# Optimization experiments

Hardware: AMD Instinct MI355X
Metric: run time of the kernel (lower is better)

The kernel has to match this reference:

```python
import jax, jax.numpy as jnp
import numpy as np

D_MODEL = 1024
NUM_HEADS = 8
D_K = D_MODEL // NUM_HEADS
NEG_INF = -1e9
EPS = 1e-6


def setup_inputs() -> dict:
    key = jax.random.key(0)
    ks = jax.random.split(key, 10)
    B, S = 4, 2048
    scale = 1.0 / np.sqrt(D_MODEL)
    return {
        "queries": jax.random.normal(ks[0], (B, S, D_MODEL), jnp.float32),
        "keys": jax.random.normal(ks[1], (B, S, D_MODEL), jnp.float32),
        "values": jax.random.normal(ks[2], (B, S, D_MODEL), jnp.float32),
        "Wq": jax.random.normal(ks[3], (D_MODEL, D_MODEL), jnp.float32) * scale,
        "bq": jnp.zeros((D_MODEL,), jnp.float32),
        "Wk": jax.random.normal(ks[4], (D_MODEL, D_MODEL), jnp.float32) * scale,
        "bk": jnp.zeros((D_MODEL,), jnp.float32),
        "Wv": jax.random.normal(ks[5], (D_MODEL, D_MODEL), jnp.float32) * scale,
        "bv": jnp.zeros((D_MODEL,), jnp.float32),
        "gamma": jnp.ones((D_MODEL,), jnp.float32),
        "beta": jnp.zeros((D_MODEL,), jnp.float32),
    }


def _split_heads(x, B, S):
    # [B,S,D] -> [B,H,S,d_k]
    return x.reshape(B, S, NUM_HEADS, D_K).transpose(0, 2, 1, 3)


def reference(queries, keys, values, Wq, bq, Wk, bk, Wv, bv, gamma, beta):
    B, S, _ = queries.shape
    Q = _split_heads(queries @ Wq + bq, B, S)
    K = _split_heads(keys @ Wk + bk, B, keys.shape[1])
    V = _split_heads(values @ Wv + bv, B, values.shape[1])
    scores = jnp.einsum("bhqd,bhkd->bhqk", Q, K) / jnp.sqrt(jnp.float32(D_K))
    # causal mask (lower triangular kept)
    Sk = scores.shape[-1]
    mask = jnp.tril(jnp.ones((scores.shape[-2], Sk), dtype=bool))
    scores = jnp.where(mask, scores, jnp.float32(NEG_INF))
    attn = jax.nn.softmax(scores, axis=-1)
    # dropout disabled (training=False)
    out = jnp.einsum("bhqk,bhkd->bhqd", attn, V)
    out = out.transpose(0, 2, 1, 3).reshape(B, S, D_MODEL)
    resid = out + queries
    mu = jnp.mean(resid, axis=-1, keepdims=True)
    var = jnp.var(resid, axis=-1, keepdims=True)
    normed = (resid - mu) / jnp.sqrt(var + EPS)
    return normed * gamma + beta
```

## Files before the change

kernel.cpp:

```cpp
#include <hip/hip_runtime.h>
#include <hip/hip_bf16.h>
#include <stdint.h>

#define D_MODEL 1024
#define S_LEN   2048
#define BATCH   4
#define NH      8
#define DK      128

typedef __attribute__((ext_vector_type(8))) __bf16 bf16x8;
typedef __attribute__((ext_vector_type(4))) float  f32x4;

__device__ __forceinline__ f32x4 mfma16(bf16x8 a, bf16x8 b, f32x4 c) {
  return __builtin_amdgcn_mfma_f32_16x16x32_bf16(a, b, c, 0, 0, 0);
}

__device__ __forceinline__ void gld_lds16(const void* g, void* l) {
  __builtin_amdgcn_global_load_lds(
      (const __attribute__((address_space(1))) void*)g,
      (__attribute__((address_space(3))) void*)l, 16, 0, 0);
}

#define ATTN_SCALE 0.08838834764831845f

__global__ __launch_bounds__(256) void prep_kernel(
    const float* __restrict__ q, const float* __restrict__ k,
    const float* __restrict__ v, const float* __restrict__ Wq,
    const float* __restrict__ Wk, const float* __restrict__ Wv,
    __hip_bfloat16* __restrict__ Xbf, __hip_bfloat16* __restrict__ Wt) {
  __shared__ __hip_bfloat16 tile[32][33];
  const int w  = blockIdx.y;
  const int tid = threadIdx.x;
  if (blockIdx.x < 8192) {
    const size_t N = (size_t)BATCH * S_LEN * D_MODEL;
    const float* src = (w == 0) ? q : (w == 1) ? k : v;
    __hip_bfloat16* dst = Xbf + (size_t)w * N;
    const size_t i = ((size_t)blockIdx.x * 256 + tid) * 4;
    const float4 vv = *(const float4*)(src + i);
    *(__hip_bfloat162*)(dst + i)     = __float22bfloat162_rn(make_float2(vv.x, vv.y));
    *(__hip_bfloat162*)(dst + i + 2) = __float22bfloat162_rn(make_float2(vv.z, vv.w));
  } else {
    const int bidx = blockIdx.x - 8192;
    const int bx = bidx & 31, by = bidx >> 5;
    const float* src = (w == 0) ? Wq : (w == 1) ? Wk : Wv;
    const float sc = (w == 0) ? ATTN_SCALE : 1.0f;
    __hip_bfloat16* dst = Wt + (size_t)w * D_MODEL * D_MODEL;
    const int tx = tid & 31, ty = tid >> 5;
    int x = bx * 32 + tx;
    int y = by * 32 + ty;
    for (int i = 0; i < 32; i += 8)
      tile[ty + i][tx] = __float2bfloat16(src[(size_t)(y + i) * D_MODEL + x] * sc);
    __syncthreads();
    x = by * 32 + tx;
    y = bx * 32 + ty;
    for (int i = 0; i < 32; i += 8)
      dst[(size_t)(y + i) * D_MODEL + x] = tile[tx][ty + i];
  }
}

__global__ __launch_bounds__(256) void qkv_gemm_kernel(
    const __hip_bfloat16* __restrict__ Xbf,
    const float* __restrict__ bq, const float* __restrict__ bk,
    const float* __restrict__ bv,
    const __hip_bfloat16* __restrict__ Wt,
    __hip_bfloat16* __restrict__ Qo, __hip_bfloat16* __restrict__ Ko,
    __hip_bfloat16* __restrict__ Vo) {
  const int flat = blockIdx.x;
  const int xcd  = flat & 7;
  const int idx  = flat >> 3;
  const int n_t  = idx & 7;
  const int mg   = idx >> 3;
  const int pair = xcd * 24 + mg;
  const int which = pair >> 6;
  const int m_t   = pair & 63;

  const size_t N = (size_t)BATCH * S_LEN * D_MODEL;
  const __hip_bfloat16* X = Xbf + (size_t)which * N;
  const __hip_bfloat16* W = Wt + (size_t)which * D_MODEL * D_MODEL;
  const float* bias = (which == 0) ? bq : (which == 1) ? bk : bv;
  const float bscale = (which == 0) ? ATTN_SCALE : 1.0f;

  __shared__ __align__(16) __hip_bfloat16 SMEM[4][128 * 64];
  __hip_bfloat16* Cb = (__hip_bfloat16*)SMEM;

  const int tid  = threadIdx.x;
  const int lane = tid & 63;
  const int wv   = tid >> 6;
  const int lo16 = lane & 15;
  const int hi4  = lane >> 4;
  const int m0 = m_t * 128;
  const int n0 = n_t * 128;
  const int wm = (wv >> 1) * 64;
  const int wn = (wv & 1) * 64;

  f32x4 acc[4][4];
  const f32x4 z4 = {0.f, 0.f, 0.f, 0.f};
  for (int i = 0; i < 4; ++i)
    for (int j = 0; j < 4; ++j) acc[i][j] = z4;

  auto stage = [&](int t, int buf) {
#pragma unroll
    for (int it = 0; it < 4; ++it) {
      const int cbase = it * 256 + wv * 64;
      const int c = cbase + lane;
      const int row = c >> 3;
      const int kc = ((c & 7) ^ (row & 7)) * 8;
      gld_lds16(X + (size_t)(m0 + row) * D_MODEL + t * 64 + kc,
                &SMEM[2 * buf][cbase * 8]);
      gld_lds16(W + (size_t)(n0 + row) * D_MODEL + t * 64 + kc,
                &SMEM[2 * buf + 1][cbase * 8]);
    }
  };

  stage(0, 0);
  int bsel = 0;
  for (int t = 0; t < 16; ++t) {
    asm volatile("s_waitcnt vmcnt(0)" ::: "memory");
    __builtin_amdgcn_s_barrier();
    asm volatile("" ::: "memory");
    if (t + 1 < 16) stage(t + 1, bsel ^ 1);

    const __hip_bfloat16* Asm = SMEM[2 * bsel];
    const __hip_bfloat16* Bsm = SMEM[2 * bsel + 1];
    for (int kk = 0; kk < 2; ++kk) {
      bf16x8 af[4], bfr[4];
      const int sl = (kk * 4 + hi4);
      for (int i = 0; i < 4; ++i) {
        const int lm = wm + 16 * i + lo16;
        af[i] = *(const bf16x8*)&Asm[lm * 64 + ((sl ^ (lm & 7)) * 8)];
      }
      for (int j = 0; j < 4; ++j) {
        const int ln = wn + 16 * j + lo16;
        bfr[j] = *(const bf16x8*)&Bsm[ln * 64 + ((sl ^ (ln & 7)) * 8)];
      }
      for (int i = 0; i < 4; ++i)
        for (int j = 0; j < 4; ++j)
          acc[i][j] = mfma16(af[i], bfr[j], acc[i][j]);
    }
    bsel ^= 1;
  }

  const int b  = m0 >> 11;
  const int s0 = m0 & (S_LEN - 1);
  const int h  = n0 >> 7;
  const size_t bh = (size_t)(b * NH + h);

  __syncthreads();
  for (int j = 0; j < 4; ++j) {
    const int nl = wn + 16 * j + lo16;
    const float bval = bias[n0 + nl] * bscale;
    for (int i = 0; i < 4; ++i) {
      for (int r = 0; r < 4; ++r) {
        const int lm = wm + 16 * i + hi4 * 4 + r;
        const __hip_bfloat16 ob = __float2bfloat16(acc[i][j][r] + bval);
        if (which == 2) {
          const int col = (lm & 96) + 2 * (lm & 15) + ((lm >> 4) & 1);
          Cb[nl * 136 + col] = ob;
        } else {
          Cb[lm * 136 + nl] = ob;
        }
      }
    }
  }
  __syncthreads();

  if (which == 0) {
    __hip_bfloat16* gq = Qo + (bh * S_LEN + s0) * DK;
    for (int r8 = 0; r8 < 8; ++r8) {
      const int C = r8 * 256 + tid;
      const bf16x8 v = *(const bf16x8*)&Cb[(C >> 4) * 136 + (C & 15) * 8];
      *(bf16x8*)&gq[(size_t)C * 8] = v;
    }
  } else if (which == 1) {
    __hip_bfloat16* gk = Ko + (bh * 64 + (s0 >> 5)) * 4096;
    for (int r8 = 0; r8 < 8; ++r8) {
      const int C = r8 * 256 + tid;
      const int su = C >> 9, Cw = C & 511;
      const bf16x8 v =
          *(const bf16x8*)&Cb[(su * 32 + (Cw & 31)) * 136 + (Cw >> 5) * 8];
      *(bf16x8*)&gk[(size_t)su * 4096 + (Cw >> 5) * 256 + (Cw & 31) * 8] = v;
    }
  } else {
    __hip_bfloat16* gv = Vo + (bh * 64 + (s0 >> 5)) * 4096;
    for (int r8 = 0; r8 < 8; ++r8) {
      const int C = r8 * 256 + tid;
      const int su = C >> 9, Cw = C & 511;
      const bf16x8 v =
          *(const bf16x8*)&Cb[(C & 127) * 136 + su * 32 + (Cw >> 7) * 8];
      *(bf16x8*)&gv[(size_t)su * 4096 + (size_t)Cw * 8] = v;
    }
  }
}

__device__ const uint32_t ATTN_TBL[24] = {
  79, 95, 32,
  78, 94, 33,
  77, 93, 34,
  76, 92, 35,
  75, 91, 36,
  39, 72, 88,
  38, 73, 89,
  37, 74, 90
};

__global__ __launch_bounds__(256, 3) void attn_kernel(
    const __hip_bfloat16* __restrict__ Qw, const __hip_bfloat16* __restrict__ Kw,
    const __hip_bfloat16* __restrict__ Vtw, __hip_bfloat16* __restrict__ Og,
    float* __restrict__ partO, float* __restrict__ lsumP) {
  const int bid = blockIdx.x;
  const int q8  = bid & 255;
  const int rr  = bid >> 8;
  const int bh  = q8 & 31;
  const int jrow = q8 >> 5;
  const int h   = bh & 7;
  const int b   = bh >> 3;
  const uint32_t wi = ATTN_TBL[jrow * 3 + rr];
  const int  t     = wi & 15;
  const int  chnk  = (wi >> 4) & 1;
  const bool split = (wi >> 5) == 2;
  const int  half  = 2 * t + 2;
  const int  st0   = (split && chnk == 1) ? half : 0;
  const int  stN   = (split && chnk == 0) ? half : (4 * t + 4);

  const int tid  = threadIdx.x;
  const int lane = tid & 63;
  const int wv   = tid >> 6;
  const int lo16 = lane & 15;
  const int hi4  = lane >> 4;

  const int qrow0 = t * 128 + wv * 32;
  const int ns_w  = 4 * t + wv + 1;

  const size_t bhp = (size_t)(b * NH + h);
  const __hip_bfloat16* Qp = Qw + bhp * S_LEN * DK;
  const __hip_bfloat16* Kp = Kw + bhp * S_LEN * DK;
  const __hip_bfloat16* Vp = Vtw + bhp * S_LEN * DK;

  __shared__ __align__(16) __hip_bfloat16 Ksm[2][32 * 128];
  __shared__ __align__(16) __hip_bfloat16 Psm[4][32 * 40];

  bf16x8 qf[2][4];
  for (int m = 0; m < 2; ++m)
    for (int kk = 0; kk < 4; ++kk)
      qf[m][kk] = *(const bf16x8*)&Qp[(size_t)(qrow0 + m * 16 + lo16) * DK +
                                      kk * 32 + hi4 * 8];

  f32x4 oacc[2][8];
  const f32x4 z4 = {0.f, 0.f, 0.f, 0.f};
  for (int m = 0; m < 2; ++m)
    for (int j = 0; j < 8; ++j) oacc[m][j] = z4;
  float lsum[2][4];
  for (int m = 0; m < 2; ++m)
    for (int i = 0; i < 4; ++i) lsum[m][i] = 0.f;

  const __hip_bfloat16* kbase[2];
#pragma unroll
  for (int it = 0; it < 2; ++it)
    kbase[it] = Kp + (size_t)(it * 256 + tid) * 8;
  auto stage = [&](int st, int buf) {
#pragma unroll
    for (int it = 0; it < 2; ++it) {
      const int cb = (it * 256 + wv * 64) * 8;
      gld_lds16(kbase[it] + ((size_t)st << 12), &Ksm[buf][cb]);
    }
  };

  stage(st0, 0);

  int bsel = 0;
  for (int st = st0; st < stN; ++st) {
    asm volatile("s_waitcnt vmcnt(0)" ::: "memory");
    __builtin_amdgcn_s_barrier();
    asm volatile("" ::: "memory");

    const bool act = st < ns_w;

    bf16x8 vf[8];
    if (act) {
      const __hip_bfloat16* vt = Vp + ((size_t)st << 12);
#pragma unroll
      for (int j = 0; j < 8; ++j)
        vf[j] = *(const bf16x8*)&vt[(hi4 * 128 + j * 16 + lo16) * 8];
    }
    if (st + 1 < stN) stage(st + 1, bsel ^ 1);

    if (act) {
      const __hip_bfloat16* Kb = Ksm[bsel];

      bf16x8 kf[2][4];
      for (int kn = 0; kn < 2; ++kn)
        for (int kk = 0; kk < 4; ++kk)
          kf[kn][kk] = *(const bf16x8*)&Kb[((kk * 4 + hi4) * 32 + kn * 16 + lo16) * 8];
      f32x4 sc[2][2];
      for (int m = 0; m < 2; ++m)
        for (int kn = 0; kn < 2; ++kn) {
          f32x4 s4 = z4;
          for (int kk = 0; kk < 4; ++kk)
            s4 = mfma16(qf[m][kk], kf[kn][kk], s4);
          sc[m][kn] = s4;
        }

      const int kv0 = st << 5;
      const bool do_mask = (st == ns_w - 1);
      for (int m = 0; m < 2; ++m) {
        for (int i = 0; i < 4; ++i) {
          const int qg = qrow0 + m * 16 + hi4 * 4 + i;
          float s0 = sc[m][0][i];
          float s1 = sc[m][1][i];
          if (do_mask) {
            if (kv0 + lo16 > qg)      s0 = -1.0e30f;
            if (kv0 + 16 + lo16 > qg) s1 = -1.0e30f;
          }
          const float p0 = __expf(s0 - 8.f);
          const float p1 = __expf(s1 - 8.f);
          lsum[m][i] += p0 + p1;
          const int prw = m * 16 + hi4 * 4 + i;
          *(__hip_bfloat162*)&Psm[wv][prw * 40 + 2 * lo16] =
              __float22bfloat162_rn(make_float2(p0, p1));
        }
      }
      asm volatile("s_waitcnt lgkmcnt(0)" ::: "memory");

      bf16x8 pf[2];
      for (int m = 0; m < 2; ++m)
        pf[m] = *(const bf16x8*)&Psm[wv][(m * 16 + lo16) * 40 + hi4 * 8];
      for (int j = 0; j < 8; ++j) {
        oacc[0][j] = mfma16(pf[0], vf[j], oacc[0][j]);
        oacc[1][j] = mfma16(pf[1], vf[j], oacc[1][j]);
      }
    }
    bsel ^= 1;
  }

  for (int m = 0; m < 2; ++m) {
    for (int i = 0; i < 4; ++i) {
      float l = lsum[m][i];
      l += __shfl_xor(l, 1);
      l += __shfl_xor(l, 2);
      l += __shfl_xor(l, 4);
      l += __shfl_xor(l, 8);
      const int row = wv * 32 + m * 16 + hi4 * 4 + i;
      if (!split) {
        const float inv = 1.0f / l;
        const int qg = t * 128 + row;
        __hip_bfloat16* orow = Og + ((size_t)b * S_LEN + qg) * D_MODEL + h * DK;
        for (int j = 0; j < 8; ++j)
          orow[j * 16 + lo16] = __float2bfloat16(oacc[m][j][i] * inv);
      } else {
        const int pidx = bh * 8 + (t - 8);
        float* prow = partO +
            (((size_t)chnk * 256 + pidx) * 128 + row) * 128;
        for (int j = 0; j < 8; ++j)
          prow[j * 16 + lo16] = oacc[m][j][i];
        if (lo16 == 0)
          lsumP[(chnk * 256 + pidx) * 128 + row] = l;
      }
    }
  }
}

__global__ __launch_bounds__(256) void ln_kernel(
    const __hip_bfloat16* __restrict__ Og, const float* __restrict__ partO,
    const float* __restrict__ lsumP, const float* __restrict__ resid_in,
    const float* __restrict__ gamma, const float* __restrict__ beta,
    float* __restrict__ out) {
  const int row  = blockIdx.x;
  const int b    = row >> 11;
  const int srow = row & (S_LEN - 1);
  const int tile = srow >> 7;
  const int tid  = threadIdx.x;
  const int base = tid * 4;
  const float4 q4 = *(const float4*)(resid_in + (size_t)row * D_MODEL + base);
  float v[4];
  if (tile < 8) {
    const __hip_bfloat16* orow = Og + (size_t)row * D_MODEL;
    const ushort4 o4 = *(const ushort4*)(orow + base);
    v[0] = __bfloat162float(*(const __hip_bfloat16*)&o4.x) + q4.x;
    v[1] = __bfloat162float(*(const __hip_bfloat16*)&o4.y) + q4.y;
    v[2] = __bfloat162float(*(const __hip_bfloat16*)&o4.z) + q4.z;
    v[3] = __bfloat162float(*(const __hip_bfloat16*)&o4.w) + q4.w;
  } else {
    const int h    = base >> 7;
    const int rin  = srow & 127;
    const int pidx = (b * 8 + h) * 8 + (tile - 8);
    const size_t off = ((size_t)pidx * 128 + rin) * 128 + (base & 127);
    const float4 p0 = *(const float4*)(partO + off);
    const float4 p1 = *(const float4*)(partO + (size_t)256 * 128 * 128 + off);
    const float l = lsumP[pidx * 128 + rin] +
                    lsumP[256 * 128 + pidx * 128 + rin];
    const float inv = 1.0f / l;
    v[0] = (p0.x + p1.x) * inv + q4.x;
    v[1] = (p0.y + p1.y) * inv + q4.y;
    v[2] = (p0.z + p1.z) * inv + q4.z;
    v[3] = (p0.w + p1.w) * inv + q4.w;
  }
  float s = v[0] + v[1] + v[2] + v[3];
  float ss = v[0] * v[0] + v[1] * v[1] + v[2] * v[2] + v[3] * v[3];
  for (int m = 1; m < 64; m <<= 1) { s += __shfl_xor(s, m); ss += __shfl_xor(ss, m); }
  __shared__ float red[8];
  const int wv = tid >> 6, lane = tid & 63;
  if (lane == 0) { red[wv] = s; red[4 + wv] = ss; }
  __syncthreads();
  s  = red[0] + red[1] + red[2] + red[3];
  ss = red[4] + red[5] + red[6] + red[7];
  const float mu  = s * (1.0f / D_MODEL);
  const float var = ss * (1.0f / D_MODEL) - mu * mu;
  const float rstd = rsqrtf(var + 1e-6f);
  const float4 g4 = *(const float4*)(gamma + base);
  const float4 b4 = *(const float4*)(beta + base);
  float4 o;
  o.x = (v[0] - mu) * rstd * g4.x + b4.x;
  o.y = (v[1] - mu) * rstd * g4.y + b4.y;
  o.z = (v[2] - mu) * rstd * g4.z + b4.z;
  o.w = (v[3] - mu) * rstd * g4.w + b4.w;
  *(float4*)(out + (size_t)row * D_MODEL + base) = o;
}

extern "C" void kernel_launch(void* const* d_in, const int* in_sizes, int n_in,
                              void* d_out, int out_size, void* d_ws, size_t ws_size,
                              hipStream_t stream) {
  const float* queries = (const float*)d_in[0];
  const float* keys    = (const float*)d_in[1];
  const float* values  = (const float*)d_in[2];
  const float* Wq = (const float*)d_in[3];
  const float* bq = (const float*)d_in[4];
  const float* Wk = (const float*)d_in[5];
  const float* bk = (const float*)d_in[6];
  const float* Wv = (const float*)d_in[7];
  const float* bv = (const float*)d_in[8];
  const float* gamma = (const float*)d_in[9];
  const float* beta  = (const float*)d_in[10];

  char* ws = (char*)d_ws;
  const size_t N = (size_t)BATCH * S_LEN * D_MODEL;
  const size_t WT_BYTES  = (size_t)3 * D_MODEL * D_MODEL * 2;
  const size_t XBF_BYTES = (size_t)3 * N * 2;
  const size_t QKV_BYTES = (size_t)BATCH * NH * S_LEN * DK * 2;
  const size_t OG_BYTES  = (size_t)BATCH * S_LEN * D_MODEL * 2;
  __hip_bfloat16* Wt  = (__hip_bfloat16*)ws;
  __hip_bfloat16* Xbf = (__hip_bfloat16*)(ws + WT_BYTES);
  __hip_bfloat16* Ogs = (__hip_bfloat16*)(ws + WT_BYTES);
  float* partO = (float*)(ws + WT_BYTES + OG_BYTES);
  float* lsumP = (float*)ws;
  __hip_bfloat16* Qws = (__hip_bfloat16*)(ws + WT_BYTES + XBF_BYTES);
  __hip_bfloat16* Kws = (__hip_bfloat16*)(ws + WT_BYTES + XBF_BYTES + QKV_BYTES);
  __hip_bfloat16* Vws = (__hip_bfloat16*)(ws + WT_BYTES + XBF_BYTES + 2 * QKV_BYTES);

  prep_kernel<<<dim3(8192 + 1024, 3), 256, 0, stream>>>(
      queries, keys, values, Wq, Wk, Wv, Xbf, Wt);
  qkv_gemm_kernel<<<dim3(1536), 256, 0, stream>>>(
      Xbf, bq, bk, bv, Wt, Qws, Kws, Vws);
  attn_kernel<<<dim3(768), 256, 0, stream>>>(Qws, Kws, Vws, Ogs, partO, lsumP);
  ln_kernel<<<dim3(BATCH * S_LEN), 256, 0, stream>>>(Ogs, partO, lsumP, queries,
                                                     gamma, beta, (float*)d_out);
}
```

Measured before the change: 315.1 us.

## Triple-buffer projection GEMM with K=32 stages and double attention KV tile size

The projection GEMM now uses three 32-wide K stages with a prefetch distance of two, waiting on vmcnt(4) instead of draining all loads each step. This keeps loads in flight across the barrier. The attention kernel stages 64 keys per barrier instead of 32, processing two 32-key halves per iteration with separate P buffers, so there are half as many barriers and waits per key. The cost is more LDS and registers (two V fragment sets), which may reduce occupancy under launch_bounds(256,3).

```diff
diff --git a/kernel.cpp b/kernel.cpp
--- a/kernel.cpp
+++ b/kernel.cpp
@@ -80,7 +80,7 @@
   const float* bias = (which == 0) ? bq : (which == 1) ? bk : bv;
   const float bscale = (which == 0) ? ATTN_SCALE : 1.0f;
 
-  __shared__ __align__(16) __hip_bfloat16 SMEM[4][128 * 64];
+  __shared__ __align__(16) __hip_bfloat16 SMEM[6][128 * 32];
   __hip_bfloat16* Cb = (__hip_bfloat16*)SMEM;
 
   const int tid  = threadIdx.x;
@@ -100,44 +100,41 @@
 
   auto stage = [&](int t, int buf) {
 #pragma unroll
-    for (int it = 0; it < 4; ++it) {
+    for (int it = 0; it < 2; ++it) {
       const int cbase = it * 256 + wv * 64;
       const int c = cbase + lane;
-      const int row = c >> 3;
-      const int kc = ((c & 7) ^ (row & 7)) * 8;
-      gld_lds16(X + (size_t)(m0 + row) * D_MODEL + t * 64 + kc,
+      const int row = c >> 2;
+      const int kc = ((c & 3) ^ (row & 3)) * 8;
+      gld_lds16(X + (size_t)(m0 + row) * D_MODEL + t * 32 + kc,
                 &SMEM[2 * buf][cbase * 8]);
-      gld_lds16(W + (size_t)(n0 + row) * D_MODEL + t * 64 + kc,
+      gld_lds16(W + (size_t)(n0 + row) * D_MODEL + t * 32 + kc,
                 &SMEM[2 * buf + 1][cbase * 8]);
     }
   };
 
   stage(0, 0);
-  int bsel = 0;
-  for (int t = 0; t < 16; ++t) {
-    asm volatile("s_waitcnt vmcnt(0)" ::: "memory");
+  stage(1, 1);
+  for (int t = 0; t < 32; ++t) {
+    if (t < 30) asm volatile("s_waitcnt vmcnt(4)" ::: "memory");
+    else        asm volatile("s_waitcnt vmcnt(0)" ::: "memory");
     __builtin_amdgcn_s_barrier();
     asm volatile("" ::: "memory");
-    if (t + 1 < 16) stage(t + 1, bsel ^ 1);
-
-    const __hip_bfloat16* Asm = SMEM[2 * bsel];
-    const __hip_bfloat16* Bsm = SMEM[2 * bsel + 1];
-    for (int kk = 0; kk < 2; ++kk) {
-      bf16x8 af[4], bfr[4];
-      const int sl = (kk * 4 + hi4);
-      for (int i = 0; i < 4; ++i) {
-        const int lm = wm + 16 * i + lo16;
-        af[i] = *(const bf16x8*)&Asm[lm * 64 + ((sl ^ (lm & 7)) * 8)];
-      }
-      for (int j = 0; j < 4; ++j) {
-        const int ln = wn + 16 * j + lo16;
-        bfr[j] = *(const bf16x8*)&Bsm[ln * 64 + ((sl ^ (ln & 7)) * 8)];
-      }
-      for (int i = 0; i < 4; ++i)
-        for (int j = 0; j < 4; ++j)
-          acc[i][j] = mfma16(af[i], bfr[j], acc[i][j]);
-    }
-    bsel ^= 1;
+    if (t + 2 < 32) stage(t + 2, (t + 2) % 3);
+
+    const __hip_bfloat16* Asm = SMEM[2 * (t % 3)];
+    const __hip_bfloat16* Bsm = SMEM[2 * (t % 3) + 1];
+    bf16x8 af[4], bfr[4];
+    for (int i = 0; i < 4; ++i) {
+      const int lm = wm + 16 * i + lo16;
+      af[i] = *(const bf16x8*)&Asm[lm * 32 + ((hi4 ^ (lm & 3)) * 8)];
+    }
+    for (int j = 0; j < 4; ++j) {
+      const int ln = wn + 16 * j + lo16;
+      bfr[j] = *(const bf16x8*)&Bsm[ln * 32 + ((hi4 ^ (ln & 3)) * 8)];
+    }
+    for (int i = 0; i < 4; ++i)
+      for (int j = 0; j < 4; ++j)
+        acc[i][j] = mfma16(af[i], bfr[j], acc[i][j]);
   }
 
   const int b  = m0 >> 11;
@@ -221,6 +218,8 @@
   const int  half  = 2 * t + 2;
   const int  st0   = (split && chnk == 1) ? half : 0;
   const int  stN   = (split && chnk == 0) ? half : (4 * t + 4);
+  const int  s0    = st0 >> 1;
+  const int  sN    = stN >> 1;
 
   const int tid  = threadIdx.x;
   const int lane = tid & 63;
@@ -236,8 +235,8 @@
   const __hip_bfloat16* Kp = Kw + bhp * S_LEN * DK;
   const __hip_bfloat16* Vp = Vtw + bhp * S_LEN * DK;
 
-  __shared__ __align__(16) __hip_bfloat16 Ksm[2][32 * 128];
-  __shared__ __align__(16) __hip_bfloat16 Psm[4][32 * 40];
+  __shared__ __align__(16) __hip_bfloat16 Ksm[2][64 * 128];
+  __shared__ __align__(16) __hip_bfloat16 Psm[4][2][32 * 40];
 
   bf16x8 qf[2][4];
   for (int m = 0; m < 2; ++m)
@@ -253,82 +252,91 @@
   for (int m = 0; m < 2; ++m)
     for (int i = 0; i < 4; ++i) lsum[m][i] = 0.f;
 
-  const __hip_bfloat16* kbase[2];
+  const __hip_bfloat16* kbase[4];
 #pragma unroll
-  for (int it = 0; it < 2; ++it)
+  for (int it = 0; it < 4; ++it)
     kbase[it] = Kp + (size_t)(it * 256 + tid) * 8;
-  auto stage = [&](int st, int buf) {
+  auto stage = [&](int s, int buf) {
 #pragma unroll
-    for (int it = 0; it < 2; ++it) {
+    for (int it = 0; it < 4; ++it) {
       const int cb = (it * 256 + wv * 64) * 8;
-      gld_lds16(kbase[it] + ((size_t)st << 12), &Ksm[buf][cb]);
+      gld_lds16(kbase[it] + ((size_t)s << 13), &Ksm[buf][cb]);
     }
   };
 
-  stage(st0, 0);
+  auto half_step = [&](const __hip_bfloat16* Kb, const bf16x8* vf,
+                       int st32, int hsel) {
+    bf16x8 kf[2][4];
+    for (int kn = 0; kn < 2; ++kn)
+      for (int kk = 0; kk < 4; ++kk)
+        kf[kn][kk] = *(const bf16x8*)&Kb[((kk * 4 + hi4) * 32 + kn * 16 + lo16) * 8];
+    f32x4 sc[2][2];
+    for (int m = 0; m < 2; ++m)
+      for (int kn = 0; kn < 2; ++kn) {
+        f32x4 s4 = z4;
+        for (int kk = 0; kk < 4; ++kk)
+          s4 = mfma16(qf[m][kk], kf[kn][kk], s4);
+        sc[m][kn] = s4;
+      }
+    const int kv0 = st32 << 5;
+    const bool do_mask = (st32 == ns_w - 1);
+    for (int m = 0; m < 2; ++m) {
+      for (int i = 0; i < 4; ++i) {
+        const int qg = qrow0 + m * 16 + hi4 * 4 + i;
+        float s0v = sc[m][0][i];
+        float s1v = sc[m][1][i];
+        if (do_mask) {
+          if (kv0 + lo16 > qg)      s0v = -1.0e30f;
+          if (kv0 + 16 + lo16 > qg) s1v = -1.0e30f;
+        }
+        const float p0 = __expf(s0v - 8.f);
+        const float p1 = __expf(s1v - 8.f);
+        lsum[m][i] += p0 + p1;
+        const int prw = m * 16 + hi4 * 4 + i;
+        *(__hip_bfloat162*)&Psm[wv][hsel][prw * 40 + 2 * lo16] =
+            __float22bfloat162_rn(make_float2(p0, p1));
+      }
+    }
+    asm volatile("s_waitcnt lgkmcnt(0)" ::: "memory");
+    bf16x8 pf[2];
+    for (int m = 0; m < 2; ++m)
+      pf[m] = *(const bf16x8*)&Psm[wv][hsel][(m * 16 + lo16) * 40 + hi4 * 8];
+    for (int j = 0; j < 8; ++j) {
+      oacc[0][j] = mfma16(pf[0], vf[j], oacc[0][j]);
+      oacc[1][j] = mfma16(pf[1], vf[j], oacc[1][j]);
+    }
+  };
+
+  stage(s0, 0);
 
   int bsel = 0;
-  for (int st = st0; st < stN; ++st) {
+  for (int s = s0; s < sN; ++s) {
     asm volatile("s_waitcnt vmcnt(0)" ::: "memory");
     __builtin_amdgcn_s_barrier();
     asm volatile("" ::: "memory");
 
-    const bool act = st < ns_w;
-
-    bf16x8 vf[8];
-    if (act) {
-      const __hip_bfloat16* vt = Vp + ((size_t)st << 12);
+    const int st32a = 2 * s, st32b = 2 * s + 1;
+    const bool act0 = st32a < ns_w;
+    const bool act1 = st32b < ns_w;
+
+    bf16x8 vf0[8], vf1[8];
+    if (act0) {
+      const __hip_bfloat16* vt = Vp + ((size_t)s << 13);
 #pragma unroll
       for (int j = 0; j < 8; ++j)
-        vf[j] = *(const bf16x8*)&vt[(hi4 * 128 + j * 16 + lo16) * 8];
-    }
-    if (st + 1 < stN) stage(st + 1, bsel ^ 1);
-
-    if (act) {
-      const __hip_bfloat16* Kb = Ksm[bsel];
-
-      bf16x8 kf[2][4];
-      for (int kn = 0; kn < 2; ++kn)
-        for (int kk = 0; kk < 4; ++kk)
-          kf[kn][kk] = *(const bf16x8*)&Kb[((kk * 4 + hi4) * 32 + kn * 16 + lo16) * 8];
-      f32x4 sc[2][2];
-      for (int m = 0; m < 2; ++m)
-        for (int kn = 0; kn < 2; ++kn) {
-          f32x4 s4 = z4;
-          for (int kk = 0; kk < 4; ++kk)
-            s4 = mfma16(qf[m][kk], kf[kn][kk], s4);
-          sc[m][kn] = s4;
-        }
-
-      const int kv0 = st << 5;
-      const bool do_mask = (st == ns_w - 1);
-      for (int m = 0; m < 2; ++m) {
-        for (int i = 0; i < 4; ++i) {
-          const int qg = qrow0 + m * 16 + hi4 * 4 + i;
-          float s0 = sc[m][0][i];
-          float s1 = sc[m][1][i];
-          if (do_mask) {
-            if (kv0 + lo16 > qg)      s0 = -1.0e30f;
-            if (kv0 + 16 + lo16 > qg) s1 = -1.0e30f;
-          }
-          const float p0 = __expf(s0 - 8.f);
-          const float p1 = __expf(s1 - 8.f);
-          lsum[m][i] += p0 + p1;
-          const int prw = m * 16 + hi4 * 4 + i;
-          *(__hip_bfloat162*)&Psm[wv][prw * 40 + 2 * lo16] =
-              __float22bfloat162_rn(make_float2(p0, p1));
-        }
-      }
-      asm volatile("s_waitcnt lgkmcnt(0)" ::: "memory");
-
-      bf16x8 pf[2];
-      for (int m = 0; m < 2; ++m)
-        pf[m] = *(const bf16x8*)&Psm[wv][(m * 16 + lo16) * 40 + hi4 * 8];
-      for (int j = 0; j < 8; ++j) {
-        oacc[0][j] = mfma16(pf[0], vf[j], oacc[0][j]);
-        oacc[1][j] = mfma16(pf[1], vf[j], oacc[1][j]);
-      }
-    }
+        vf0[j] = *(const bf16x8*)&vt[(hi4 * 128 + j * 16 + lo16) * 8];
+    }
+    if (act1) {
+      const __hip_bfloat16* vt = Vp + ((size_t)s << 13) + 4096;
+#pragma unroll
+      for (int j = 0; j < 8; ++j)
+        vf1[j] = *(const bf16x8*)&vt[(hi4 * 128 + j * 16 + lo16) * 8];
+    }
+    if (s + 1 < sN) stage(s + 1, bsel ^ 1);
+
+    const __hip_bfloat16* Kb = Ksm[bsel];
+    if (act0) half_step(Kb, vf0, st32a, 0);
+    if (act1) half_step(Kb + 4096, vf1, st32b, 1);
     bsel ^= 1;
   }
 
```

Result: slower. 455.8 us (+44.7%).
